# Optimization experiments

Measured on AMD Instinct MI355X. Metric: run time of the kernel, lower is better.

## Reference

```python
import jax, jax.numpy as jnp
import numpy as np

NUM_CODES = 1024
HIDDEN = 256
BETA = 0.25


def setup_inputs() -> dict:
    key = jax.random.key(0)
    k1, k2 = jax.random.split(key)
    z = jax.random.normal(k1, (16, 256, 64, 64), dtype=jnp.float32)
    # torch init: uniform(-1/K, 1/K)
    codebook = jax.random.uniform(
        k2, (NUM_CODES, HIDDEN), dtype=jnp.float32,
        minval=-1.0 / NUM_CODES, maxval=1.0 / NUM_CODES)
    return {"z": z, "codebook": codebook}


def reference(z, codebook):
    # z: [B, C, H, W] -> [B, H, W, C]
    z_nhwc = jnp.transpose(z, (0, 2, 3, 1))
    B, H, W, D = z_nhwc.shape
    zf = z_nhwc.reshape(-1, D)  # [N, D]
    # pairwise squared distances: ||z||^2 + ||e||^2 - 2 z e^T  -> [N, K]
    d = (jnp.sum(zf * zf, axis=1, keepdims=True)
         + jnp.sum(codebook * codebook, axis=1)
         - 2.0 * jnp.matmul(zf, codebook.T))
    idx = jnp.argmin(d, axis=1)  # [N]
    z_q = codebook[idx].reshape(B, H, W, D)
    sg = jax.lax.stop_gradient
    loss = (jnp.mean((sg(z_q) - z_nhwc) ** 2)
            + BETA * jnp.mean((z_q - sg(z_nhwc)) ** 2))
    # straight-through estimator
    z_q = z_nhwc + sg(z_q - z_nhwc)
    z_q = jnp.transpose(z_q, (0, 3, 1, 2))  # back to NCHW
    return z_q, idx, loss
```

## Files before the change

### kernel.cpp

```cpp
#include <hip/hip_runtime.h>
#include <hip/hip_bf16.h>

#define NCODES 1024
#define DIMS   256
#define HWSZ   4096
#define NPOS   65536

#define TN 128
#define TK 128
#define CC 16
#define NKC (NCODES / TK)
#define NCC (DIMS / CC)

#define WS_LOSS 0
#define WS_B    256
#define WS_A    2048
#define WS_CBT  67584

__global__ void prep_kernel(const float* __restrict__ cb, float* __restrict__ ws) {
#pragma clang fp contract(off)
    int k = blockIdx.x * blockDim.x + threadIdx.x;
    if (k == 0) ws[WS_LOSS] = 0.0f;
    float* bsum = ws + WS_B;
    float* cbT  = ws + WS_CBT;
    if (k < NCODES) {
        float s = 0.0f;
        for (int c = 0; c < DIMS; ++c) {
            float v = cb[k * DIMS + c];
            float p = v * v;
            s = s + p;
            cbT[c * NCODES + k] = v;
        }
        bsum[k] = s;
    }
}

__global__ void a_kernel(const float* __restrict__ z, float* __restrict__ ws) {
#pragma clang fp contract(off)
    int n = blockIdx.x * blockDim.x + threadIdx.x;
    int b = n >> 12;
    int hw = n & 4095;
    const float* zp = z + (size_t)b * DIMS * HWSZ + hw;
    float s = 0.0f;
    for (int c = 0; c < DIMS; ++c) {
        float v = zp[(size_t)c * HWSZ];
        float p = v * v;
        s = s + p;
    }
    ws[WS_A + n] = s;
}

__global__ __launch_bounds__(256, 4)
void vq_main(const float* __restrict__ z, const float* __restrict__ cb,
             float* __restrict__ ws, float* __restrict__ out) {
    __shared__ __align__(16) char smem[33792];
    float* zs    = (float*)smem;
    float* cbs   = (float*)(smem + 8192);
    float* red_d = (float*)(smem + 16384);
    int*   red_i = (int*)(smem + 24576);
    float* es    = (float*)smem;
    int*   bi_s  = (int*)(smem + 32768);
    float* a_s   = (float*)(smem + 33280);

    const float* bsum = ws + WS_B;
    const float* a_g  = ws + WS_A;
    const float* cbT  = ws + WS_CBT;

    const int t  = threadIdx.x;
    const int ti = t & 15;
    const int tj = t >> 4;

    const int n0  = blockIdx.x * TN;
    const int b   = n0 >> 12;
    const int hw0 = n0 & 4095;
    const size_t zb = (size_t)b * DIMS * HWSZ;

    if (t < TN) a_s[t] = a_g[n0 + t];

    float run_d = 1e30f;
    int   run_i = 0;

    for (int kc = 0; kc < NKC; ++kc) {
        const int k0 = kc * TK;
        float acc[8][8];
#pragma unroll
        for (int i = 0; i < 8; ++i)
#pragma unroll
            for (int j = 0; j < 8; ++j) acc[i][j] = 0.0f;

        for (int ccI = 0; ccI < NCC; ++ccI) {
            const int c0 = ccI * CC;
            __syncthreads();
#pragma unroll
            for (int issue = 0; issue < 2; ++issue) {
                int f   = issue * 1024 + t * 4;
                int cl  = f >> 7;
                int col = f & 127;
                float4 v = *(const float4*)(z + zb + (size_t)(c0 + cl) * HWSZ + hw0 + col);
                *(float4*)(zs + cl * TN + col) = v;
            }
#pragma unroll
            for (int issue = 0; issue < 2; ++issue) {
                int f   = issue * 1024 + t * 4;
                int cl  = f >> 7;
                int col = f & 127;
                float4 v = *(const float4*)(cbT + (size_t)(c0 + cl) * NCODES + k0 + col);
                *(float4*)(cbs + cl * TK + col) = v;
            }
            __syncthreads();
#pragma unroll
            for (int c = 0; c < CC; ++c) {
                const float4 za  = *(const float4*)(zs + c * TN + ti * 4);
                const float4 zb4 = *(const float4*)(zs + c * TN + 64 + ti * 4);
                const float4 ca  = *(const float4*)(cbs + c * TK + tj * 8);
                const float4 cb4 = *(const float4*)(cbs + c * TK + tj * 8 + 4);
                float zr[8] = {za.x, za.y, za.z, za.w, zb4.x, zb4.y, zb4.z, zb4.w};
                float cr[8] = {ca.x, ca.y, ca.z, ca.w, cb4.x, cb4.y, cb4.z, cb4.w};
#pragma unroll
                for (int i = 0; i < 8; ++i)
#pragma unroll
                    for (int j = 0; j < 8; ++j)
                        acc[i][j] = fmaf(zr[i], cr[j], acc[i][j]);
            }
        }

        float bfrag[8];
#pragma unroll
        for (int j = 0; j < 8; ++j) bfrag[j] = bsum[k0 + tj * 8 + j];

        __syncthreads();
#pragma unroll
        for (int i = 0; i < 8; ++i) {
            const int nl = (i < 4) ? (ti * 4 + i) : (64 + ti * 4 + (i - 4));
            const float an = a_s[nl];
            float bd = 1e30f;
            int   bi = 0;
#pragma unroll
            for (int j = 0; j < 8; ++j) {
                const int kk = k0 + tj * 8 + j;
                float t1 = an + bfrag[j];
                float d  = t1 - 2.0f * acc[i][j];
                if (d < bd) { bd = d; bi = kk; }
            }
            red_d[nl * 16 + tj] = bd;
            red_i[nl * 16 + tj] = bi;
        }
        __syncthreads();
        if (t < TN) {
#pragma unroll 4
            for (int tj2 = 0; tj2 < 16; ++tj2) {
                float d2 = red_d[t * 16 + tj2];
                int   i2 = red_i[t * 16 + tj2];
                if (d2 < run_d) { run_d = d2; run_i = i2; }
            }
        }
    }

    if (t < TN) {
        bi_s[t] = run_i;
        out[(size_t)NPOS * DIMS + n0 + t] = (float)run_i;
    }

    float lpart = 0.0f;
    for (int pass = 0; pass < 4; ++pass) {
        const int tp = pass * 32;
        __syncthreads();
        for (int rr = 0; rr < 32; ++rr) {
            const int idx = bi_s[tp + rr];
            es[rr * 256 + (t ^ rr)] = cb[(size_t)idx * DIMS + t];
        }
        __syncthreads();
#pragma unroll 4
        for (int r2 = 0; r2 < 32; ++r2) {
            const int fl2 = r2 * 256 + t;
            const int c   = fl2 >> 5;
            const int tnl = fl2 & 31;
            const float e = es[tnl * 256 + (c ^ tnl)];
            const size_t gz = zb + (size_t)c * HWSZ + hw0 + tp + tnl;
            const float zv = z[gz];
            const float diff = e - zv;
            lpart = fmaf(diff, diff, lpart);
            out[gz] = zv + diff;
        }
    }

    for (int off = 32; off > 0; off >>= 1)
        lpart += __shfl_down(lpart, off);
    if ((t & 63) == 0) a_s[t >> 6] = lpart;
    __syncthreads();
    if (t == 0) {
        float s = a_s[0] + a_s[1] + a_s[2] + a_s[3];
        atomicAdd(ws + WS_LOSS, s);
    }
}

__global__ void loss_final(const float* __restrict__ ws, float* __restrict__ out) {
    float m = ws[WS_LOSS] / 16777216.0f;
    out[(size_t)NPOS * DIMS + NPOS] = m + 0.25f * m;
}

extern "C" void kernel_launch(void* const* d_in, const int* in_sizes, int n_in,
                              void* d_out, int out_size, void* d_ws, size_t ws_size,
                              hipStream_t stream) {
    (void)in_sizes; (void)n_in; (void)out_size; (void)ws_size;
    const float* z  = (const float*)d_in[0];
    const float* cb = (const float*)d_in[1];
    float* ws  = (float*)d_ws;
    float* out = (float*)d_out;

    prep_kernel<<<4, 256, 0, stream>>>(cb, ws);
    a_kernel<<<NPOS / 256, 256, 0, stream>>>(z, ws);
    vq_main<<<NPOS / TN, 256, 0, stream>>>(z, cb, ws, out);
    loss_final<<<1, 1, 0, stream>>>(ws, out);
}
```

Measured before the change: 820.3 us.

## Use split-bf16 MFMA distance search with near-tie FP32 rescue pass

Replaces the FP32 SIMT distance GEMM with bf16 MFMA. Both z and the codebook are split into high and low bf16 parts (three-term products) and pre-packed into MFMA-friendly layouts in workspace. Each row tracks its best and second-best distance, and rows whose gap is below a threshold are queued for an exact FP32 rescan so argmin matches the reference. The gather, straight-through output and loss become a separate pass with deterministic per-block partial sums. This adds prep kernels and a large workspace, and the path runs only if the workspace is large enough.

```diff
diff --git a/kernel.cpp b/kernel.cpp
--- a/kernel.cpp
+++ b/kernel.cpp
@@ -5,13 +5,330 @@
 #define DIMS   256
 #define HWSZ   4096
 #define NPOS   65536
+
+__device__ __forceinline__ unsigned short f2bf_rne(float f) {
+    unsigned int x = __float_as_uint(f);
+    unsigned int r = x + 0x7fffu + ((x >> 16) & 1u);
+    return (unsigned short)(r >> 16);
+}
+__device__ __forceinline__ float bf2f(unsigned short h) {
+    return __uint_as_float(((unsigned int)h) << 16);
+}
+__device__ __forceinline__ void gl_lds16(const void* g, void* l) {
+    __builtin_amdgcn_global_load_lds(
+        (const __attribute__((address_space(1))) unsigned int*)g,
+        (__attribute__((address_space(3))) unsigned int*)l, 16, 0, 0);
+}
+
+typedef short bf16x8v __attribute__((ext_vector_type(8)));
+typedef float f32x4  __attribute__((ext_vector_type(4)));
+
+#define WM_CNT   0
+#define WM_PART  64
+#define WM_B     1024
+#define WM_A     2048
+#define WM_IDX   67584
+#define WM_LIST  133120
+#define WM_BM    198656
+#define WM_AM    591872
+#define WM_END_BYTES 69476352ull
+#define THRESH 2.5e-4f
+
+__global__ void prep_cb_m(const float* __restrict__ cb, float* __restrict__ ws) {
+#pragma clang fp contract(off)
+    int k = blockIdx.x * 256 + threadIdx.x;
+    if (k == 0) ((int*)ws)[WM_CNT] = 0;
+    float s = 0.0f;
+    for (int c = 0; c < DIMS; ++c) {
+        float v = cb[k * DIMS + c];
+        float p = v * v;
+        s = s + p;
+    }
+    ws[WM_B + k] = s;
+
+    unsigned short* Bm = (unsigned short*)(ws + WM_BM);
+    const int kc = k >> 8, cg = (k >> 4) & 15, c16 = k & 15;
+    for (int ci = 0; ci < 24; ++ci) {
+        const int base = (ci < 8 ? ci : (ci < 16 ? ci - 8 : ci - 16)) * 32;
+        const bool lo = (ci >= 8 && ci < 16);
+        for (int q = 0; q < 4; ++q) {
+            union { unsigned short u[8]; uint4 v4; } pk;
+#pragma unroll
+            for (int j = 0; j < 8; ++j) {
+                float v = cb[k * DIMS + base + q * 8 + j];
+                unsigned short h = f2bf_rne(v);
+                if (lo) h = f2bf_rne(v - bf2f(h));
+                pk.u[j] = h;
+            }
+            size_t off = ((size_t)(((kc * 24 + ci) * 16 + cg) * 4 + q)) * 128 + c16 * 8;
+            *(uint4*)(Bm + off) = pk.v4;
+        }
+    }
+}
+
+__global__ void prep_a_m(const float* __restrict__ z, float* __restrict__ ws) {
+#pragma clang fp contract(off)
+    int n = blockIdx.x * blockDim.x + threadIdx.x;
+    int b = n >> 12;
+    int hw = n & 4095;
+    const float* zp = z + (size_t)b * DIMS * HWSZ + hw;
+    float s = 0.0f;
+    for (int c = 0; c < DIMS; ++c) {
+        float v = zp[(size_t)c * HWSZ];
+        float p = v * v;
+        s = s + p;
+    }
+    ws[WM_A + n] = s;
+}
+
+__global__ __launch_bounds__(256)
+void prep_zsplit(const float* __restrict__ z, float* __restrict__ ws) {
+    __shared__ float lz[128 * 64];
+    unsigned short* Am = (unsigned short*)(ws + WM_AM);
+    const int t = threadIdx.x;
+    const int tile = blockIdx.x;
+    const int n0 = tile * 64;
+    const int b = n0 >> 12, hw0 = n0 & 4095;
+    const size_t zbase = (size_t)b * DIMS * HWSZ + hw0;
+    const int p = t & 63, grp = t >> 6;
+    unsigned short* At = Am + (size_t)tile * 32768;
+
+    for (int half = 0; half < 2; ++half) {
+        const int coff = half * 128;
+        __syncthreads();
+        for (int rep = 0; rep < 32; ++rep) {
+            int cl = rep * 4 + grp;
+            lz[cl * 64 + p] = z[zbase + (size_t)(coff + cl) * HWSZ + p];
+        }
+        __syncthreads();
+        for (int run = 0; run < 4; ++run) {
+            const int c0l = grp * 32 + run * 8;
+            union { unsigned short u[8]; uint4 v4; } hh, ll;
+#pragma unroll
+            for (int j = 0; j < 8; ++j) {
+                float v = lz[(c0l + j) * 64 + p];
+                unsigned short h = f2bf_rne(v);
+                hh.u[j] = h;
+                ll.u[j] = f2bf_rne(v - bf2f(h));
+            }
+            const int kp = (coff >> 5) + grp;
+            const size_t byteH = (size_t)kp * 4096 +
+                                 (size_t)((p >> 4) * 4 + run) * 256 + (p & 15) * 16;
+            *(uint4*)((char*)At + byteH)         = hh.v4;
+            *(uint4*)((char*)At + byteH + 32768) = ll.v4;
+        }
+    }
+}
+
+__global__ __launch_bounds__(256, 4)
+void vq_mfma_k(const float* __restrict__ ws_ro, float* __restrict__ ws) {
+    __shared__ char Al[4096];
+    __shared__ char Bl[16384];
+    __shared__ float rd1[256], rd2[256];
+    __shared__ int   ri[256];
+
+    const int t = threadIdx.x, w = t >> 6, lane = t & 63;
+    const int rg = lane >> 4, cl = lane & 15;
+    const int tile = blockIdx.x, n0 = tile * 64;
+
+    const unsigned short* Am = (const unsigned short*)(ws_ro + WM_AM);
+    const unsigned short* Bm = (const unsigned short*)(ws_ro + WM_BM);
+    const float* bsum = ws_ro + WM_B;
+    const char* Atile = (const char*)(Am + (size_t)tile * 32768);
+
+    rd1[t] = 1e30f; rd2[t] = 1e30f; ri[t] = 0;
+
+    for (int kc = 0; kc < 4; ++kc) {
+        f32x4 acc[4][4];
+#pragma unroll
+        for (int g = 0; g < 4; ++g)
+#pragma unroll
+            for (int bb = 0; bb < 4; ++bb)
+#pragma unroll
+                for (int r = 0; r < 4; ++r) acc[g][bb][r] = 0.0f;
+
+        for (int ci = 0; ci < 24; ++ci) {
+            __syncthreads();
+            const int kp = (ci < 8) ? ci : ci - 8;
+            gl_lds16(Atile + (size_t)kp * 4096 + t * 16, Al + (t & ~63) * 16);
+            const char* Bci = (const char*)Bm + (size_t)(kc * 24 + ci) * 16384;
+#pragma unroll
+            for (int i = 0; i < 4; ++i)
+                gl_lds16(Bci + (size_t)(i * 256 + t) * 16,
+                         Bl + i * 4096 + (t & ~63) * 16);
+            __syncthreads();
+
+            bf16x8v af[4], bfv[4];
+#pragma unroll
+            for (int g = 0; g < 4; ++g)
+                af[g] = *(const bf16x8v*)(Al + (g * 4 + rg) * 256 + cl * 16);
+#pragma unroll
+            for (int bb = 0; bb < 4; ++bb)
+                bfv[bb] = *(const bf16x8v*)(Bl + ((w * 4 + bb) * 4 + rg) * 256 + cl * 16);
+#pragma unroll
+            for (int g = 0; g < 4; ++g)
+#pragma unroll
+                for (int bb = 0; bb < 4; ++bb)
+                    acc[g][bb] = __builtin_amdgcn_mfma_f32_16x16x32_bf16(
+                        af[g], bfv[bb], acc[g][bb], 0, 0, 0);
+        }
+
+        const int cwbase = kc * 256 + w * 64;
+        float bs[4];
+#pragma unroll
+        for (int bb = 0; bb < 4; ++bb) bs[bb] = bsum[cwbase + bb * 16 + cl];
+
+#pragma unroll
+        for (int g = 0; g < 4; ++g) {
+#pragma unroll
+            for (int r = 0; r < 4; ++r) {
+                float d1 = 1e30f, d2 = 1e30f; int i1 = 0;
+#pragma unroll
+                for (int bb = 0; bb < 4; ++bb) {
+                    float s = fmaf(-2.0f, acc[g][bb][r], bs[bb]);
+                    int kk = cwbase + bb * 16 + cl;
+                    if (s < d1) { d2 = d1; d1 = s; i1 = kk; }
+                    else if (s < d2) d2 = s;
+                }
+#pragma unroll
+                for (int off = 1; off < 16; off <<= 1) {
+                    float o1 = __shfl_xor(d1, off);
+                    float o2 = __shfl_xor(d2, off);
+                    int   oi = __shfl_xor(i1, off);
+                    float nm = fminf(fmaxf(d1, o1), fminf(d2, o2));
+                    bool take = (o1 < d1) || (o1 == d1 && oi < i1);
+                    d1 = take ? o1 : d1; i1 = take ? oi : i1; d2 = nm;
+                }
+                if (cl == 0) {
+                    int slot = w * 64 + g * 16 + rg * 4 + r;
+                    float o1 = rd1[slot], o2 = rd2[slot];
+                    if (d1 < o1) { ri[slot] = i1; rd1[slot] = d1; rd2[slot] = fminf(o1, d2); }
+                    else          rd2[slot] = fminf(o2, d1);
+                }
+            }
+        }
+    }
+
+    __syncthreads();
+    if (t < 64) {
+        float d1 = rd1[t], d2 = rd2[t]; int i1 = ri[t];
+#pragma unroll
+        for (int ww = 1; ww < 4; ++ww) {
+            float o1 = rd1[ww * 64 + t], o2 = rd2[ww * 64 + t];
+            int   oi = ri[ww * 64 + t];
+            if (o1 < d1) { d2 = fminf(d1, o2); d1 = o1; i1 = oi; }
+            else          d2 = fminf(d2, o1);
+        }
+        ((int*)ws)[WM_IDX + n0 + t] = i1;
+        if (d2 - d1 < THRESH) {
+            int slot = atomicAdd((int*)ws + WM_CNT, 1);
+            ((int*)ws)[WM_LIST + slot] = n0 + t;
+        }
+    }
+}
+
+__global__ void rescue_k(const float* __restrict__ z, const float* __restrict__ cb,
+                         float* __restrict__ ws) {
+#pragma clang fp contract(off)
+    const int t = threadIdx.x, lane = t & 63;
+    const int wslot = blockIdx.x * 4 + (t >> 6);
+    const int cnt = ((const int*)ws)[WM_CNT];
+    for (int i = wslot; i < cnt; i += 1024) {
+        const int row = ((const int*)ws)[WM_LIST + i];
+        const int b = row >> 12, hw = row & 4095;
+        const float* zp = z + (size_t)b * DIMS * HWSZ + hw;
+        const float a = ws[WM_A + row];
+        float d1 = 1e30f; int i1 = 0;
+        for (int j = 0; j < 16; ++j) {
+            const int kk = lane * 16 + j;
+            const float* cr = cb + (size_t)kk * DIMS;
+            float acc = 0.0f;
+            for (int c4 = 0; c4 < 64; ++c4) {
+                float4 cv = *(const float4*)(cr + c4 * 4);
+                acc = fmaf(zp[(size_t)(c4 * 4 + 0) * HWSZ], cv.x, acc);
+                acc = fmaf(zp[(size_t)(c4 * 4 + 1) * HWSZ], cv.y, acc);
+                acc = fmaf(zp[(size_t)(c4 * 4 + 2) * HWSZ], cv.z, acc);
+                acc = fmaf(zp[(size_t)(c4 * 4 + 3) * HWSZ], cv.w, acc);
+            }
+            float t1 = a + ws[WM_B + kk];
+            float d  = t1 - 2.0f * acc;
+            if (d < d1) { d1 = d; i1 = kk; }
+        }
+#pragma unroll
+        for (int off = 1; off < 64; off <<= 1) {
+            float od = __shfl_xor(d1, off);
+            int   oi = __shfl_xor(i1, off);
+            bool take = (od < d1) || (od == d1 && oi < i1);
+            d1 = take ? od : d1; i1 = take ? oi : i1;
+        }
+        if (lane == 0) ((int*)ws)[WM_IDX + row] = i1;
+    }
+}
+
+__global__ __launch_bounds__(256)
+void pass3_k(const float* __restrict__ z, const float* __restrict__ cb,
+             float* __restrict__ ws, float* __restrict__ out) {
+    __shared__ float es[32 * 256];
+    __shared__ int   bi_s[128];
+    __shared__ float wred[4];
+    const int t = threadIdx.x;
+    const int n0 = blockIdx.x * 128;
+    const int b = n0 >> 12, hw0 = n0 & 4095;
+    const size_t zb = (size_t)b * DIMS * HWSZ;
+
+    if (t < 128) bi_s[t] = ((const int*)ws)[WM_IDX + n0 + t];
+
+    float lpart = 0.0f;
+    for (int pass = 0; pass < 4; ++pass) {
+        const int tp = pass * 32;
+        __syncthreads();
+        for (int rr = 0; rr < 32; ++rr) {
+            const int idx = bi_s[tp + rr];
+            es[rr * 256 + (t ^ rr)] = cb[(size_t)idx * DIMS + t];
+        }
+        __syncthreads();
+#pragma unroll 4
+        for (int r2 = 0; r2 < 32; ++r2) {
+            const int fl2 = r2 * 256 + t;
+            const int c   = fl2 >> 5;
+            const int tnl = fl2 & 31;
+            const float e = es[tnl * 256 + (c ^ tnl)];
+            const size_t gz = zb + (size_t)c * HWSZ + hw0 + tp + tnl;
+            const float zv = z[gz];
+            const float diff = e - zv;
+            lpart = fmaf(diff, diff, lpart);
+            out[gz] = zv + diff;
+        }
+    }
+    if (t < 128) out[(size_t)NPOS * DIMS + n0 + t] = (float)bi_s[t];
+
+    for (int off = 32; off > 0; off >>= 1) lpart += __shfl_down(lpart, off);
+    if ((t & 63) == 0) wred[t >> 6] = lpart;
+    __syncthreads();
+    if (t == 0)
+        ws[WM_PART + blockIdx.x] = wred[0] + wred[1] + wred[2] + wred[3];
+}
+
+__global__ void loss_final_m(const float* __restrict__ ws, float* __restrict__ out) {
+    __shared__ float ls[64];
+    const int t = threadIdx.x;
+    float s = 0.0f;
+    for (int i = 0; i < 8; ++i) s += ws[WM_PART + t * 8 + i];
+    ls[t] = s;
+    __syncthreads();
+    if (t == 0) {
+        float tot = 0.0f;
+        for (int i = 0; i < 64; ++i) tot += ls[i];
+        float m = tot / 16777216.0f;
+        out[(size_t)NPOS * DIMS + NPOS] = m + 0.25f * m;
+    }
+}
 
 #define TN 128
 #define TK 128
 #define CC 16
 #define NKC (NCODES / TK)
 #define NCC (DIMS / CC)
-
 #define WS_LOSS 0
 #define WS_B    256
 #define WS_A    2048
@@ -202,14 +519,24 @@
 extern "C" void kernel_launch(void* const* d_in, const int* in_sizes, int n_in,
                               void* d_out, int out_size, void* d_ws, size_t ws_size,
                               hipStream_t stream) {
-    (void)in_sizes; (void)n_in; (void)out_size; (void)ws_size;
+    (void)in_sizes; (void)n_in; (void)out_size;
     const float* z  = (const float*)d_in[0];
     const float* cb = (const float*)d_in[1];
     float* ws  = (float*)d_ws;
     float* out = (float*)d_out;
 
-    prep_kernel<<<4, 256, 0, stream>>>(cb, ws);
-    a_kernel<<<NPOS / 256, 256, 0, stream>>>(z, ws);
-    vq_main<<<NPOS / TN, 256, 0, stream>>>(z, cb, ws, out);
-    loss_final<<<1, 1, 0, stream>>>(ws, out);
-}
+    if (ws_size >= WM_END_BYTES) {
+        prep_cb_m<<<4, 256, 0, stream>>>(cb, ws);
+        prep_a_m<<<NPOS / 256, 256, 0, stream>>>(z, ws);
+        prep_zsplit<<<1024, 256, 0, stream>>>(z, ws);
+        vq_mfma_k<<<1024, 256, 0, stream>>>(ws, ws);
+        rescue_k<<<256, 256, 0, stream>>>(z, cb, ws);
+        pass3_k<<<512, 256, 0, stream>>>(z, cb, ws, out);
+        loss_final_m<<<1, 64, 0, stream>>>(ws, out);
+    } else {
+        prep_kernel<<<4, 256, 0, stream>>>(cb, ws);
+        a_kernel<<<NPOS / 256, 256, 0, stream>>>(z, ws);
+        vq_main<<<NPOS / TN, 256, 0, stream>>>(z, cb, ws, out);
+        loss_final<<<1, 1, 0, stream>>>(ws, out);
+    }
+}
```

After: 984.5 us. 20.0% more time.
